# Performance work log

Measured on AMD Instinct MI355X. Metric: run time of the kernel, lower is better.

The kernel has to match this reference:

```python
import jax, jax.numpy as jnp
import numpy as np

N0, N1, N2, N3, N4, C = 65536, 16384, 4096, 1024, 256, 256


def _linear_params(key, fan_in, fan_out):
    kw, kb = jax.random.split(key)
    lim = 1.0 / np.sqrt(fan_in)
    W = jax.random.uniform(kw, (fan_in, fan_out), minval=-lim, maxval=lim, dtype=jnp.float32)
    b = jax.random.uniform(kb, (fan_out,), minval=-lim, maxval=lim, dtype=jnp.float32)
    return W, b


def setup_inputs() -> dict:
    key = jax.random.key(0)
    ks = jax.random.split(key, 20)
    inp = {
        'xyz0': jax.random.normal(ks[0], (N0, 3), dtype=jnp.float32),
        'idx0': jax.random.randint(ks[1], (N0,), 0, N1),
        'idx1': jax.random.randint(ks[2], (N1,), 0, N0),
        'idx2': jax.random.randint(ks[3], (N2,), 0, N0),
        'idx3': jax.random.randint(ks[4], (N3,), 0, N0),
        'idx4': jax.random.randint(ks[5], (N4,), 0, N0),
    }
    names = ['W_all', 'b_all', 'W4', 'b4', 'W3', 'b3', 'W2', 'b2', 'W1', 'b1', 'W0', 'b0']
    for i in range(6):
        W, b = _linear_params(ks[6 + i], 3, C)
        inp[names[2 * i]] = W
        inp[names[2 * i + 1]] = b
    pnames = ['P4', 'pb4', 'P3', 'pb3', 'P2', 'pb2', 'P1', 'pb1', 'P0', 'pb0']
    for i in range(5):
        W, b = _linear_params(ks[12 + i], 2 * C, C)
        inp[pnames[2 * i]] = W
        inp[pnames[2 * i + 1]] = b
    return inp


def _nn1(xyz, new_xyz):
    # global 1-NN (single batch segment): argmin of squared distance
    d = (jnp.sum(new_xyz ** 2, -1, keepdims=True)
         - 2.0 * new_xyz @ xyz.T
         + jnp.sum(xyz ** 2, -1))  # [M, N]
    return jnp.argmin(d, axis=1)


def _fwd(xyz0, idx0, idx1, idx2, idx3, idx4,
         W_all, b_all, W4, b4, W3, b3, W2, b2, W1, b1, W0, b0,
         P4, pb4, P3, pb3, P2, pb2, P1, pb1, P0, pb0):
    xyz4 = xyz0[idx4]
    xyz3 = xyz0[idx3]
    xyz2 = xyz0[idx2]
    xyz1 = xyz0[idx1]
    f0 = xyz0 @ W_all + b_all          # [N0, C]
    f1, f2, f3, f4 = f0[:N1], f0[:N2], f0[:N3], f0[:N4]
    # level 4: global max pooling as class token (single-batch scatter-amax)
    cls4 = jnp.max(f4, axis=0, keepdims=True)  # [1, C], broadcasts over N4
    f4_nei = cls4 + (xyz4 @ W4 + b4)
    pe4 = jnp.concatenate([f4_nei, f4], axis=-1) @ P4 + pb4
    # level 3
    k34 = _nn1(xyz4, xyz3)
    f3_nei = pe4[k34] + ((xyz3 - xyz4[k34]) @ W3 + b3)
    pe3 = jnp.concatenate([f3_nei, f3], axis=-1) @ P3 + pb3
    # level 2
    k23 = _nn1(xyz3, xyz2)
    f2_nei = pe3[k23] + ((xyz2 - xyz3[k23]) @ W2 + b2)
    pe2 = jnp.concatenate([f2_nei, f2], axis=-1) @ P2 + pb2
    # level 1
    k12 = _nn1(xyz2, xyz1)
    f1_nei = pe2[k12] + ((xyz1 - xyz2[k12]) @ W1 + b1)
    pe1 = jnp.concatenate([f1_nei, f1], axis=-1) @ P1 + pb1
    # level 0: precomputed indices into level 1
    f0_nei = pe1[idx0] + ((xyz0 - xyz1[idx0]) @ W0 + b0)
    pe0 = jnp.concatenate([f0_nei, f0], axis=-1) @ P0 + pb0
    return (pe4, pe3, pe2, pe1, pe0)


def reference(xyz0, idx0, idx1, idx2, idx3, idx4,
              W_all, b_all, W4, b4, W3, b3, W2, b2, W1, b1, W0, b0,
              P4, pb4, P3, pb3, P2, pb2, P1, pb1, P0, pb0):
    return _fwd(xyz0, idx0, idx1, idx2, idx3, idx4,
                W_all, b_all, W4, b4, W3, b3, W2, b2, W1, b1, W0, b0,
                P4, pb4, P3, pb3, P2, pb2, P1, pb1, P0, pb0)
```

## Files before the change

kernel.cpp:

```cpp
#include <hip/hip_runtime.h>
#include <hip/hip_bf16.h>


typedef __hip_bfloat16 bf16;
typedef unsigned short ushort_t;
typedef __attribute__((ext_vector_type(8))) short short8;
typedef __attribute__((ext_vector_type(4))) float float4v;

#define cN0 65536
#define cN1 16384
#define cN2 4096
#define cN3 1024
#define cN4 256

__device__ __forceinline__ float b2f(bf16 v) { return __bfloat162float(v); }

__device__ __forceinline__ ushort_t f2b(float v) {
    union { float f; unsigned u; } x; x.f = v;
    unsigned r = x.u + 0x7FFF + ((x.u >> 16) & 1);
    return (ushort_t)(r >> 16);
}

__global__ void detect_kernel(const unsigned short* __restrict__ raw, int* __restrict__ flag) {
    __shared__ int bad;
    if (threadIdx.x == 0) bad = 0;
    __syncthreads();
    for (int i = threadIdx.x; i < 1024; i += 256) {
        int e = (raw[i] >> 7) & 0xFF;
        if (e >= 138) atomicOr(&bad, 1);
    }
    __syncthreads();
    if (threadIdx.x == 0) flag[0] = bad ? 1 : 0;
}

struct CanonArgs { const void* src[23]; };

__global__ void canon_kernel(CanonArgs a, const int* __restrict__ flag, float* __restrict__ dst) {
    const int sizes[23] = {196608, 768, 256,
                           768, 256, 768, 256, 768, 256, 768, 256, 768, 256,
                           131072, 256, 131072, 256, 131072, 256, 131072, 256, 131072, 256};
    int fp32 = flag[0];
    int gid = blockIdx.x * 256 + threadIdx.x;
    int off = 0;
#pragma unroll
    for (int s = 0; s < 23; ++s) {
        int n = sizes[s];
        if (gid >= off && gid < off + n) {
            int local = gid - off;
            float v = fp32 ? ((const float*)a.src[s])[local]
                           : b2f(((const bf16*)a.src[s])[local]);
            dst[gid] = v;
        }
        off += n;
    }
}

__global__ void prep_kernel(const float* __restrict__ Pbase, const float* __restrict__ Wbase,
                            const float* __restrict__ Wallf, const float* __restrict__ ballf,
                            const float* __restrict__ xyzf,
                            ushort_t* __restrict__ PTb,
                            float* __restrict__ M1, float* __restrict__ M2,
                            float* __restrict__ cbuf) {
    __shared__ __align__(16) char smem[16640];
    int bidx = blockIdx.x;
    int tid = threadIdx.x;

    if (bidx < 80) {
        int level = bidx >> 4;
        int kb = (bidx >> 2) & 3;
        int nb = bidx & 3;
        const float* P = Pbase + (size_t)level * 131328;
        ushort_t* PT = PTb + (size_t)level * 65536;
        float (*tile)[65] = (float (*)[65])smem;
        int tx = tid & 63, ty = tid >> 6;
        for (int r = ty; r < 64; r += 4)
            tile[r][tx] = P[(size_t)(kb * 64 + r) * 256 + nb * 64 + tx];
        __syncthreads();
        for (int r = ty; r < 64; r += 4)
            PT[(size_t)(nb * 64 + r) * 256 + kb * 64 + tx] = f2b(tile[tx][r]);
        return;
    }

    int L = (bidx - 80) >> 3;
    int tb = (bidx - 80) & 7;
    const float* P = Pbase + (size_t)L * 131328;
    const float* W = Wbase + (size_t)L * 1024;
    const float* b = W + 768;
    const float* pb = P + 131072;

    float* cls4f = (float*)smem;
    float* red = (float*)(smem + 1024);
    float* px = (float*)(smem + 1024 + 7168);
    float* py = px + 256;
    float* pz = py + 256;

    if (L == 0) {
        px[tid] = xyzf[3 * tid + 0];
        py[tid] = xyzf[3 * tid + 1];
        pz[tid] = xyzf[3 * tid + 2];
        __syncthreads();
        float w0 = Wallf[tid], w1 = Wallf[256 + tid], w2 = Wallf[512 + tid];
        float bb = ballf[tid];
        float best = -3.402823466e38f;
        for (int i = 0; i < 256; ++i) {
            float v = fmaf(pz[i], w2, fmaf(py[i], w1, px[i] * w0)) + bb;
            best = fmaxf(best, v);
        }
        cls4f[tid] = best;
        __syncthreads();
    }

    int j = tid & 31;
    int slice = tid >> 5;
    int col = tb * 32 + j;

    float m10 = 0.f, m11 = 0.f, m12 = 0.f, m20 = 0.f, m21 = 0.f, m22 = 0.f, cc = 0.f;
#pragma unroll 4
    for (int i = 0; i < 32; ++i) {
        int c = slice * 32 + i;
        float pt = P[(size_t)c * 256 + col];
        float pbot = P[(size_t)(256 + c) * 256 + col];
        m10 = fmaf(W[c], pt, m10);
        m11 = fmaf(W[256 + c], pt, m11);
        m12 = fmaf(W[512 + c], pt, m12);
        m20 = fmaf(Wallf[c], pbot, m20);
        m21 = fmaf(Wallf[256 + c], pbot, m21);
        m22 = fmaf(Wallf[512 + c], pbot, m22);
        cc = fmaf(b[c], pt, cc);
        cc = fmaf(ballf[c], pbot, cc);
        if (L == 0) cc = fmaf(cls4f[c], pt, cc);
    }

    red[0 * 256 + tid] = m10; red[1 * 256 + tid] = m11; red[2 * 256 + tid] = m12;
    red[3 * 256 + tid] = m20; red[4 * 256 + tid] = m21; red[5 * 256 + tid] = m22;
    red[6 * 256 + tid] = cc;
    __syncthreads();
    if (tid < 32) {
        float v[7];
#pragma unroll
        for (int q = 0; q < 7; ++q) {
            float s = red[q * 256 + tid];
#pragma unroll
            for (int sl = 1; sl < 8; ++sl) s += red[q * 256 + sl * 32 + tid];
            v[q] = s;
        }
        M1[(size_t)L * 768 + col] = v[0];
        M1[(size_t)L * 768 + 256 + col] = v[1];
        M1[(size_t)L * 768 + 512 + col] = v[2];
        M2[(size_t)L * 768 + col] = v[3];
        M2[(size_t)L * 768 + 256 + col] = v[4];
        M2[(size_t)L * 768 + 512 + col] = v[5];
        cbuf[(size_t)L * 256 + col] = v[6] + pb[col];
    }
}

__device__ __forceinline__ void nn_body(const float* __restrict__ xyzf,
                                        const int* __restrict__ idxQ,
                                        const int* __restrict__ idxR, int nR,
                                        int* __restrict__ outK, int blk,
                                        float4* ref4, float* redD, int* redI) {
    int tid = threadIdx.x;
    int part = tid >> 6;
    int q = blk * 64 + (tid & 63);
    int qi = idxQ[q];
    float qx = xyzf[3 * qi + 0];
    float qy = xyzf[3 * qi + 1];
    float qz = xyzf[3 * qi + 2];
    float q2 = (qx * qx + qy * qy) + qz * qz;
    float best = 3.402823466e38f;
    int bi = 0;
    for (int base = 0; base < nR; base += 1024) {
        int nt = min(1024, nR - base);
        __syncthreads();
        for (int t = tid; t < nt; t += 256) {
            int ri = idxR[base + t];
            float x = xyzf[3 * ri + 0];
            float y = xyzf[3 * ri + 1];
            float z = xyzf[3 * ri + 2];
            ref4[t] = make_float4(x, y, z, (x * x + y * y) + z * z);
        }
        __syncthreads();
        int seg = nt >> 2;
        int s0 = part * seg;
        for (int t = 0; t < seg; ++t) {
            float4 rp = ref4[s0 + t];
            float dot = (qx * rp.x + qy * rp.y) + qz * rp.z;
            float d = (q2 - 2.0f * dot) + rp.w;
            if (d < best) { best = d; bi = base + s0 + t; }
        }
    }
    redD[tid] = best;
    redI[tid] = bi;
    __syncthreads();
    if (part == 0) {
#pragma unroll
        for (int p = 1; p < 4; ++p) {
            float d = redD[tid + p * 64];
            int i2 = redI[tid + p * 64];
            if (d < best || (d == best && i2 < bi)) { best = d; bi = i2; }
        }
        outK[q] = bi;
    }
}

__global__ void nn_merged(const float* __restrict__ xyzf,
                          const int* __restrict__ idx1, const int* __restrict__ idx2,
                          const int* __restrict__ idx3, const int* __restrict__ idx4,
                          int* __restrict__ k34, int* __restrict__ k23,
                          int* __restrict__ k12) {
    __shared__ __align__(16) float4 ref4[1024];
    __shared__ float redD[256];
    __shared__ int redI[256];
    int b = blockIdx.x;
    if (b < 16)       nn_body(xyzf, idx3, idx4, cN4, k34, b, ref4, redD, redI);
    else if (b < 80)  nn_body(xyzf, idx2, idx3, cN3, k23, b - 16, ref4, redD, redI);
    else              nn_body(xyzf, idx1, idx2, cN2, k12, b - 80, ref4, redD, redI);
}

__global__ void pe4_kernel(const float* __restrict__ xyzf, const int* __restrict__ idx4,
                           const float* __restrict__ M1, const float* __restrict__ M2,
                           const float* __restrict__ cbuf, const int* __restrict__ flag,
                           void* __restrict__ outv, ushort_t* __restrict__ peB) {
    int row = blockIdx.x;
    int n = threadIdx.x;
    int qi = idx4[row];
    float qx = xyzf[3 * qi + 0], qy = xyzf[3 * qi + 1], qz = xyzf[3 * qi + 2];
    float xx = xyzf[3 * row + 0], yy = xyzf[3 * row + 1], zz = xyzf[3 * row + 2];
    float v = cbuf[n];
    v = fmaf(qx, M1[n], v);
    v = fmaf(qy, M1[256 + n], v);
    v = fmaf(qz, M1[512 + n], v);
    v = fmaf(xx, M2[n], v);
    v = fmaf(yy, M2[256 + n], v);
    v = fmaf(zz, M2[512 + n], v);
    size_t idx = (size_t)row * 256 + n;
    if (flag[0]) ((float*)outv)[idx] = v;
    else         ((bf16*)outv)[idx] = __float2bfloat16(v);
    peB[idx] = f2b(v);
}

__global__ __launch_bounds__(256, 2) void level_mfma(
    const float* __restrict__ xyzf,
    const ushort_t* __restrict__ peB_prev,
    const int* __restrict__ kmap,
    const int* __restrict__ idxQ,
    const int* __restrict__ idxR,
    const float* __restrict__ M1, const float* __restrict__ M2,
    const float* __restrict__ cvec,
    const ushort_t* __restrict__ PT,
    const int* __restrict__ flag, void* __restrict__ outv, size_t out_off,
    ushort_t* __restrict__ peB_out) {
    __shared__ float m1l[768], m2l[768], cl[256];
    __shared__ float rowD[64][3], rowX[64][3];
    __shared__ int rowK[64];
    __shared__ __align__(16) ushort_t A_lds[64 * 264];

    int tid = threadIdx.x;
    int row0 = blockIdx.x * 64;
    int fp32out = flag[0];

    for (int i = tid; i < 768; i += 256) { m1l[i] = M1[i]; m2l[i] = M2[i]; }
    cl[tid] = cvec[tid];
    if (tid < 64) {
        int r = tid, row = row0 + r;
        float xx = xyzf[3 * row + 0];
        float yy = xyzf[3 * row + 1];
        float zz = xyzf[3 * row + 2];
        rowX[r][0] = xx; rowX[r][1] = yy; rowX[r][2] = zz;
        int k = kmap[row];
        rowK[r] = k;
        float qx = xx, qy = yy, qz = zz;
        if (idxQ) {
            int qi = idxQ[row];
            qx = xyzf[3 * qi + 0];
            qy = xyzf[3 * qi + 1];
            qz = xyzf[3 * qi + 2];
        }
        int ri = idxR[k];
        float rx = xyzf[3 * ri + 0];
        float ry = xyzf[3 * ri + 1];
        float rz = xyzf[3 * ri + 2];
        rowD[r][0] = qx - rx; rowD[r][1] = qy - ry; rowD[r][2] = qz - rz;
    }
    __syncthreads();

#pragma unroll
    for (int it = 0; it < 8; ++it) {
        int lin = it * 256 + tid;
        int r = lin >> 5, ch = lin & 31;
        *(uint4*)&A_lds[r * 264 + ch * 8] =
            *(const uint4*)(peB_prev + (size_t)rowK[r] * 256 + ch * 8);
    }
    __syncthreads();

    int wave = tid >> 6;
    int lane = tid & 63;
    int quad = lane >> 4;
    int l16 = lane & 15;
    int wc = wave * 64;

    const ushort_t* bbase[4];
#pragma unroll
    for (int nt = 0; nt < 4; ++nt)
        bbase[nt] = PT + (size_t)(wc + nt * 16 + l16) * 256 + quad * 8;

    float4v acc[4][4];
#pragma unroll
    for (int mt = 0; mt < 4; ++mt)
#pragma unroll
        for (int nt = 0; nt < 4; ++nt) acc[mt][nt] = (float4v){0.f, 0.f, 0.f, 0.f};

#pragma unroll
    for (int kt = 0; kt < 8; ++kt) {
        int c0 = kt * 32;
        short8 afr[4], bfr[4];
#pragma unroll
        for (int nt = 0; nt < 4; ++nt)
            bfr[nt] = *(const short8*)(bbase[nt] + c0);
#pragma unroll
        for (int mt = 0; mt < 4; ++mt)
            afr[mt] = *(const short8*)&A_lds[(mt * 16 + l16) * 264 + c0 + quad * 8];
#pragma unroll
        for (int mt = 0; mt < 4; ++mt)
#pragma unroll
            for (int nt = 0; nt < 4; ++nt)
                acc[mt][nt] = __builtin_amdgcn_mfma_f32_16x16x32_bf16(
                    afr[mt], bfr[nt], acc[mt][nt], 0, 0, 0);
    }

#pragma unroll
    for (int mt = 0; mt < 4; ++mt) {
#pragma unroll
        for (int reg = 0; reg < 4; ++reg) {
            int rl = mt * 16 + quad * 4 + reg;
            float d0 = rowD[rl][0], d1 = rowD[rl][1], d2 = rowD[rl][2];
            float x0 = rowX[rl][0], x1 = rowX[rl][1], x2 = rowX[rl][2];
            int row = row0 + rl;
#pragma unroll
            for (int nt = 0; nt < 4; ++nt) {
                int col = wc + nt * 16 + l16;
                float v = acc[mt][nt][reg] + cl[col];
                v = fmaf(d0, m1l[col], v);
                v = fmaf(d1, m1l[256 + col], v);
                v = fmaf(d2, m1l[512 + col], v);
                v = fmaf(x0, m2l[col], v);
                v = fmaf(x1, m2l[256 + col], v);
                v = fmaf(x2, m2l[512 + col], v);
                size_t idx = (size_t)row * 256 + col;
                if (fp32out) ((float*)outv)[out_off + idx] = v;
                else         ((bf16*)outv)[out_off + idx] = __float2bfloat16(v);
                if (peB_out) peB_out[idx] = f2b(v);
            }
        }
    }
}

extern "C" void kernel_launch(void* const* d_in, const int* in_sizes, int n_in,
                              void* d_out, int out_size, void* d_ws, size_t ws_size,
                              hipStream_t stream) {
    const int* idx0 = (const int*)d_in[1];
    const int* idx1 = (const int*)d_in[2];
    const int* idx2 = (const int*)d_in[3];
    const int* idx3 = (const int*)d_in[4];
    const int* idx4 = (const int*)d_in[5];

    float* ws = (float*)d_ws;
    int* flag = (int*)ws;
    float* p = ws + 64;
    float* xyzf = p;  p += 196608;
    float* Wallf = p; p += 768;
    float* ballf = p; p += 256;
    float* Wf0 = p;   p += 5 * 1024;
    float* Pf0 = p;   p += 5 * 131328;
    float* M1buf = p; p += 5 * 768;
    float* M2buf = p; p += 5 * 768;
    float* cbuf = p;  p += 5 * 256;
    int* k34 = (int*)p; p += 1024;
    int* k23 = (int*)p; p += 4096;
    int* k12 = (int*)p; p += 16384;
    ushort_t* pe4B = (ushort_t*)p; p += 32768;
    ushort_t* pe3B = (ushort_t*)p; p += 131072;
    ushort_t* pe2B = (ushort_t*)p; p += 524288;
    ushort_t* pe1B = (ushort_t*)p; p += 2097152;
    ushort_t* PTb = (ushort_t*)p;

    detect_kernel<<<1, 256, 0, stream>>>((const unsigned short*)d_in[0], flag);

    CanonArgs ca;
    ca.src[0] = d_in[0];
    ca.src[1] = d_in[6];
    ca.src[2] = d_in[7];
    for (int i = 0; i < 10; ++i) ca.src[3 + i] = d_in[8 + i];
    for (int i = 0; i < 10; ++i) ca.src[13 + i] = d_in[18 + i];
    canon_kernel<<<3357, 256, 0, stream>>>(ca, flag, ws + 64);

    prep_kernel<<<120, 256, 0, stream>>>(Pf0, Wf0, Wallf, ballf, xyzf,
                                         PTb, M1buf, M2buf, cbuf);
    nn_merged<<<336, 256, 0, stream>>>(xyzf, idx1, idx2, idx3, idx4, k34, k23, k12);

    const size_t o4 = 0;
    const size_t o3 = (size_t)cN4 * 256;
    const size_t o2 = o3 + (size_t)cN3 * 256;
    const size_t o1 = o2 + (size_t)cN2 * 256;
    const size_t o0 = o1 + (size_t)cN1 * 256;

    pe4_kernel<<<cN4, 256, 0, stream>>>(xyzf, idx4, M1buf, M2buf, cbuf, flag, d_out, pe4B);

    level_mfma<<<cN3 / 64, 256, 0, stream>>>(
        xyzf, pe4B, k34, idx3, idx4, M1buf + 768, M2buf + 768, cbuf + 256,
        PTb + 1 * 65536, flag, d_out, o3, pe3B);
    level_mfma<<<cN2 / 64, 256, 0, stream>>>(
        xyzf, pe3B, k23, idx2, idx3, M1buf + 2 * 768, M2buf + 2 * 768, cbuf + 2 * 256,
        PTb + 2 * 65536, flag, d_out, o2, pe2B);
    level_mfma<<<cN1 / 64, 256, 0, stream>>>(
        xyzf, pe2B, k12, idx1, idx2, M1buf + 3 * 768, M2buf + 3 * 768, cbuf + 3 * 256,
        PTb + 3 * 65536, flag, d_out, o1, pe1B);
    level_mfma<<<cN0 / 64, 256, 0, stream>>>(
        xyzf, pe1B, idx0, nullptr, idx1, M1buf + 4 * 768, M2buf + 4 * 768, cbuf + 4 * 256,
        PTb + 4 * 65536, flag, d_out, o0, nullptr);
}
```

Before: 290.1 us.

## Fuse detect, prep, NN and pe4 stages into fewer kernel launches

Folds the dtype-detect step into the canonicalisation kernel, so each block recomputes the flag locally instead of running a separate one-block launch. It merges the prep and nearest-neighbour kernels into one 512-thread launch and widens the NN search from 4 to 8 partitions per query. The pe4 kernel is absorbed into a level-3 kernel that recomputes the pe4 rows it gathers on the fly, which drops the pe4 bf16 buffer and one launch. The aim is to cut launch count and serial dependencies, at the cost of redundant recomputation and half-idle threads in the prep branches.

```diff
diff --git a/kernel.cpp b/kernel.cpp
--- a/kernel.cpp
+++ b/kernel.cpp
@@ -21,26 +21,26 @@
     return (ushort_t)(r >> 16);
 }
 
-__global__ void detect_kernel(const unsigned short* __restrict__ raw, int* __restrict__ flag) {
+struct CanonArgs { const void* src[23]; };
+
+__global__ void canon_kernel(CanonArgs a, int* __restrict__ flag, float* __restrict__ dst) {
     __shared__ int bad;
-    if (threadIdx.x == 0) bad = 0;
-    __syncthreads();
-    for (int i = threadIdx.x; i < 1024; i += 256) {
+    int tid = threadIdx.x;
+    if (tid == 0) bad = 0;
+    __syncthreads();
+    const unsigned short* raw = (const unsigned short*)a.src[0];
+    for (int i = tid; i < 1024; i += 256) {
         int e = (raw[i] >> 7) & 0xFF;
         if (e >= 138) atomicOr(&bad, 1);
     }
     __syncthreads();
-    if (threadIdx.x == 0) flag[0] = bad ? 1 : 0;
-}
-
-struct CanonArgs { const void* src[23]; };
-
-__global__ void canon_kernel(CanonArgs a, const int* __restrict__ flag, float* __restrict__ dst) {
+    int fp32 = bad ? 1 : 0;
+    int gid = blockIdx.x * 256 + tid;
+    if (gid == 0) flag[0] = fp32;
+
     const int sizes[23] = {196608, 768, 256,
                            768, 256, 768, 256, 768, 256, 768, 256, 768, 256,
                            131072, 256, 131072, 256, 131072, 256, 131072, 256, 131072, 256};
-    int fp32 = flag[0];
-    int gid = blockIdx.x * 256 + threadIdx.x;
     int off = 0;
 #pragma unroll
     for (int s = 0; s < 23; ++s) {
@@ -55,104 +55,6 @@
     }
 }
 
-__global__ void prep_kernel(const float* __restrict__ Pbase, const float* __restrict__ Wbase,
-                            const float* __restrict__ Wallf, const float* __restrict__ ballf,
-                            const float* __restrict__ xyzf,
-                            ushort_t* __restrict__ PTb,
-                            float* __restrict__ M1, float* __restrict__ M2,
-                            float* __restrict__ cbuf) {
-    __shared__ __align__(16) char smem[16640];
-    int bidx = blockIdx.x;
-    int tid = threadIdx.x;
-
-    if (bidx < 80) {
-        int level = bidx >> 4;
-        int kb = (bidx >> 2) & 3;
-        int nb = bidx & 3;
-        const float* P = Pbase + (size_t)level * 131328;
-        ushort_t* PT = PTb + (size_t)level * 65536;
-        float (*tile)[65] = (float (*)[65])smem;
-        int tx = tid & 63, ty = tid >> 6;
-        for (int r = ty; r < 64; r += 4)
-            tile[r][tx] = P[(size_t)(kb * 64 + r) * 256 + nb * 64 + tx];
-        __syncthreads();
-        for (int r = ty; r < 64; r += 4)
-            PT[(size_t)(nb * 64 + r) * 256 + kb * 64 + tx] = f2b(tile[tx][r]);
-        return;
-    }
-
-    int L = (bidx - 80) >> 3;
-    int tb = (bidx - 80) & 7;
-    const float* P = Pbase + (size_t)L * 131328;
-    const float* W = Wbase + (size_t)L * 1024;
-    const float* b = W + 768;
-    const float* pb = P + 131072;
-
-    float* cls4f = (float*)smem;
-    float* red = (float*)(smem + 1024);
-    float* px = (float*)(smem + 1024 + 7168);
-    float* py = px + 256;
-    float* pz = py + 256;
-
-    if (L == 0) {
-        px[tid] = xyzf[3 * tid + 0];
-        py[tid] = xyzf[3 * tid + 1];
-        pz[tid] = xyzf[3 * tid + 2];
-        __syncthreads();
-        float w0 = Wallf[tid], w1 = Wallf[256 + tid], w2 = Wallf[512 + tid];
-        float bb = ballf[tid];
-        float best = -3.402823466e38f;
-        for (int i = 0; i < 256; ++i) {
-            float v = fmaf(pz[i], w2, fmaf(py[i], w1, px[i] * w0)) + bb;
-            best = fmaxf(best, v);
-        }
-        cls4f[tid] = best;
-        __syncthreads();
-    }
-
-    int j = tid & 31;
-    int slice = tid >> 5;
-    int col = tb * 32 + j;
-
-    float m10 = 0.f, m11 = 0.f, m12 = 0.f, m20 = 0.f, m21 = 0.f, m22 = 0.f, cc = 0.f;
-#pragma unroll 4
-    for (int i = 0; i < 32; ++i) {
-        int c = slice * 32 + i;
-        float pt = P[(size_t)c * 256 + col];
-        float pbot = P[(size_t)(256 + c) * 256 + col];
-        m10 = fmaf(W[c], pt, m10);
-        m11 = fmaf(W[256 + c], pt, m11);
-        m12 = fmaf(W[512 + c], pt, m12);
-        m20 = fmaf(Wallf[c], pbot, m20);
-        m21 = fmaf(Wallf[256 + c], pbot, m21);
-        m22 = fmaf(Wallf[512 + c], pbot, m22);
-        cc = fmaf(b[c], pt, cc);
-        cc = fmaf(ballf[c], pbot, cc);
-        if (L == 0) cc = fmaf(cls4f[c], pt, cc);
-    }
-
-    red[0 * 256 + tid] = m10; red[1 * 256 + tid] = m11; red[2 * 256 + tid] = m12;
-    red[3 * 256 + tid] = m20; red[4 * 256 + tid] = m21; red[5 * 256 + tid] = m22;
-    red[6 * 256 + tid] = cc;
-    __syncthreads();
-    if (tid < 32) {
-        float v[7];
-#pragma unroll
-        for (int q = 0; q < 7; ++q) {
-            float s = red[q * 256 + tid];
-#pragma unroll
-            for (int sl = 1; sl < 8; ++sl) s += red[q * 256 + sl * 32 + tid];
-            v[q] = s;
-        }
-        M1[(size_t)L * 768 + col] = v[0];
-        M1[(size_t)L * 768 + 256 + col] = v[1];
-        M1[(size_t)L * 768 + 512 + col] = v[2];
-        M2[(size_t)L * 768 + col] = v[3];
-        M2[(size_t)L * 768 + 256 + col] = v[4];
-        M2[(size_t)L * 768 + 512 + col] = v[5];
-        cbuf[(size_t)L * 256 + col] = v[6] + pb[col];
-    }
-}
 
 __device__ __forceinline__ void nn_body(const float* __restrict__ xyzf,
                                         const int* __restrict__ idxQ,
@@ -172,7 +74,7 @@
     for (int base = 0; base < nR; base += 1024) {
         int nt = min(1024, nR - base);
         __syncthreads();
-        for (int t = tid; t < nt; t += 256) {
+        for (int t = tid; t < nt; t += 512) {
             int ri = idxR[base + t];
             float x = xyzf[3 * ri + 0];
             float y = xyzf[3 * ri + 1];
@@ -180,7 +82,7 @@
             ref4[t] = make_float4(x, y, z, (x * x + y * y) + z * z);
         }
         __syncthreads();
-        int seg = nt >> 2;
+        int seg = nt >> 3;
         int s0 = part * seg;
         for (int t = 0; t < seg; ++t) {
             float4 rp = ref4[s0 + t];
@@ -194,7 +96,7 @@
     __syncthreads();
     if (part == 0) {
 #pragma unroll
-        for (int p = 1; p < 4; ++p) {
+        for (int p = 1; p < 8; ++p) {
             float d = redD[tid + p * 64];
             int i2 = redI[tid + p * 64];
             if (d < best || (d == best && i2 < bi)) { best = d; bi = i2; }
@@ -203,40 +105,279 @@
     }
 }
 
-__global__ void nn_merged(const float* __restrict__ xyzf,
-                          const int* __restrict__ idx1, const int* __restrict__ idx2,
-                          const int* __restrict__ idx3, const int* __restrict__ idx4,
-                          int* __restrict__ k34, int* __restrict__ k23,
-                          int* __restrict__ k12) {
-    __shared__ __align__(16) float4 ref4[1024];
-    __shared__ float redD[256];
-    __shared__ int redI[256];
+__global__ void prep_nn_kernel(const float* __restrict__ Pbase, const float* __restrict__ Wbase,
+                               const float* __restrict__ Wallf, const float* __restrict__ ballf,
+                               const float* __restrict__ xyzf,
+                               const int* __restrict__ idx1, const int* __restrict__ idx2,
+                               const int* __restrict__ idx3, const int* __restrict__ idx4,
+                               ushort_t* __restrict__ PTb,
+                               float* __restrict__ M1, float* __restrict__ M2,
+                               float* __restrict__ cbuf,
+                               int* __restrict__ k34, int* __restrict__ k23,
+                               int* __restrict__ k12) {
+    __shared__ __align__(16) char smem[20608];
     int b = blockIdx.x;
-    if (b < 16)       nn_body(xyzf, idx3, idx4, cN4, k34, b, ref4, redD, redI);
-    else if (b < 80)  nn_body(xyzf, idx2, idx3, cN3, k23, b - 16, ref4, redD, redI);
-    else              nn_body(xyzf, idx1, idx2, cN2, k12, b - 80, ref4, redD, redI);
-}
-
-__global__ void pe4_kernel(const float* __restrict__ xyzf, const int* __restrict__ idx4,
-                           const float* __restrict__ M1, const float* __restrict__ M2,
-                           const float* __restrict__ cbuf, const int* __restrict__ flag,
-                           void* __restrict__ outv, ushort_t* __restrict__ peB) {
-    int row = blockIdx.x;
-    int n = threadIdx.x;
-    int qi = idx4[row];
-    float qx = xyzf[3 * qi + 0], qy = xyzf[3 * qi + 1], qz = xyzf[3 * qi + 2];
-    float xx = xyzf[3 * row + 0], yy = xyzf[3 * row + 1], zz = xyzf[3 * row + 2];
-    float v = cbuf[n];
-    v = fmaf(qx, M1[n], v);
-    v = fmaf(qy, M1[256 + n], v);
-    v = fmaf(qz, M1[512 + n], v);
-    v = fmaf(xx, M2[n], v);
-    v = fmaf(yy, M2[256 + n], v);
-    v = fmaf(zz, M2[512 + n], v);
-    size_t idx = (size_t)row * 256 + n;
-    if (flag[0]) ((float*)outv)[idx] = v;
-    else         ((bf16*)outv)[idx] = __float2bfloat16(v);
-    peB[idx] = f2b(v);
+    int tid = threadIdx.x;
+
+    if (b < 80) {
+        int level = b >> 4;
+        int kb = (b >> 2) & 3;
+        int nb = b & 3;
+        const float* P = Pbase + (size_t)level * 131328;
+        ushort_t* PT = PTb + (size_t)level * 65536;
+        float (*tile)[65] = (float (*)[65])smem;
+        int tx = tid & 63, ty = tid >> 6;
+        for (int r = ty; r < 64; r += 8)
+            tile[r][tx] = P[(size_t)(kb * 64 + r) * 256 + nb * 64 + tx];
+        __syncthreads();
+        for (int r = ty; r < 64; r += 8)
+            PT[(size_t)(nb * 64 + r) * 256 + kb * 64 + tx] = f2b(tile[tx][r]);
+        return;
+    }
+
+    if (b < 120) {
+        int L = (b - 80) >> 3;
+        int tb = (b - 80) & 7;
+        const float* P = Pbase + (size_t)L * 131328;
+        const float* W = Wbase + (size_t)L * 1024;
+        const float* bvec = W + 768;
+        const float* pb = P + 131072;
+        float* cls4f = (float*)smem;
+        float* red = (float*)(smem + 1024);
+        float* px = (float*)(smem + 1024 + 7168);
+        float* py = px + 256;
+        float* pz = py + 256;
+
+        if (L == 0) {
+            if (tid < 256) {
+                px[tid] = xyzf[3 * tid + 0];
+                py[tid] = xyzf[3 * tid + 1];
+                pz[tid] = xyzf[3 * tid + 2];
+            }
+            __syncthreads();
+            if (tid < 256) {
+                float w0 = Wallf[tid], w1 = Wallf[256 + tid], w2 = Wallf[512 + tid];
+                float bb = ballf[tid];
+                float best = -3.402823466e38f;
+                for (int i = 0; i < 256; ++i) {
+                    float v = fmaf(pz[i], w2, fmaf(py[i], w1, px[i] * w0)) + bb;
+                    best = fmaxf(best, v);
+                }
+                cls4f[tid] = best;
+            }
+            __syncthreads();
+        }
+
+        if (tid < 256) {
+            int j = tid & 31;
+            int slice = tid >> 5;
+            int col = tb * 32 + j;
+            float m10 = 0.f, m11 = 0.f, m12 = 0.f, m20 = 0.f, m21 = 0.f, m22 = 0.f, cc = 0.f;
+#pragma unroll 4
+            for (int i = 0; i < 32; ++i) {
+                int c = slice * 32 + i;
+                float pt = P[(size_t)c * 256 + col];
+                float pbot = P[(size_t)(256 + c) * 256 + col];
+                m10 = fmaf(W[c], pt, m10);
+                m11 = fmaf(W[256 + c], pt, m11);
+                m12 = fmaf(W[512 + c], pt, m12);
+                m20 = fmaf(Wallf[c], pbot, m20);
+                m21 = fmaf(Wallf[256 + c], pbot, m21);
+                m22 = fmaf(Wallf[512 + c], pbot, m22);
+                cc = fmaf(bvec[c], pt, cc);
+                cc = fmaf(ballf[c], pbot, cc);
+                if (L == 0) cc = fmaf(cls4f[c], pt, cc);
+            }
+            red[0 * 256 + tid] = m10; red[1 * 256 + tid] = m11; red[2 * 256 + tid] = m12;
+            red[3 * 256 + tid] = m20; red[4 * 256 + tid] = m21; red[5 * 256 + tid] = m22;
+            red[6 * 256 + tid] = cc;
+        }
+        __syncthreads();
+        if (tid < 32) {
+            int col = tb * 32 + tid;
+            float v[7];
+#pragma unroll
+            for (int q = 0; q < 7; ++q) {
+                float s = red[q * 256 + tid];
+#pragma unroll
+                for (int sl = 1; sl < 8; ++sl) s += red[q * 256 + sl * 32 + tid];
+                v[q] = s;
+            }
+            M1[(size_t)L * 768 + col] = v[0];
+            M1[(size_t)L * 768 + 256 + col] = v[1];
+            M1[(size_t)L * 768 + 512 + col] = v[2];
+            M2[(size_t)L * 768 + col] = v[3];
+            M2[(size_t)L * 768 + 256 + col] = v[4];
+            M2[(size_t)L * 768 + 512 + col] = v[5];
+            cbuf[(size_t)L * 256 + col] = v[6] + pb[col];
+        }
+        return;
+    }
+
+    int blk = b - 120;
+    float4* ref4 = (float4*)smem;
+    float* redD = (float*)(smem + 16384);
+    int* redI = (int*)(smem + 18432);
+    if (blk < 16)       nn_body(xyzf, idx3, idx4, cN4, k34, blk, ref4, redD, redI);
+    else if (blk < 80)  nn_body(xyzf, idx2, idx3, cN3, k23, blk - 16, ref4, redD, redI);
+    else                nn_body(xyzf, idx1, idx2, cN2, k12, blk - 80, ref4, redD, redI);
+}
+
+__global__ __launch_bounds__(256, 2) void level3_kernel(
+    const float* __restrict__ xyzf,
+    const int* __restrict__ idx3, const int* __restrict__ idx4,
+    const int* __restrict__ k34,
+    const float* __restrict__ M1_0, const float* __restrict__ M2_0,
+    const float* __restrict__ c0,
+    const float* __restrict__ M1_1, const float* __restrict__ M2_1,
+    const float* __restrict__ c1,
+    const ushort_t* __restrict__ PT,
+    const int* __restrict__ flag, void* __restrict__ outv,
+    size_t o4, size_t o3, ushort_t* __restrict__ peB_out) {
+    __shared__ float m1l[768], m2l[768], cl[256];
+    __shared__ float rowD[64][3], rowX[64][3], refQ[64][3], refK[64][3];
+    __shared__ int rowK[64];
+    __shared__ __align__(16) ushort_t A_lds[64 * 264];
+
+    int tid = threadIdx.x;
+    int b = blockIdx.x;
+    int fp32out = flag[0];
+
+    if (b >= 16) {
+        int rows0 = (b - 16) * 64;
+        if (tid < 64) {
+            int k = rows0 + tid;
+            int qi = idx4[k];
+            refQ[tid][0] = xyzf[3 * qi + 0];
+            refQ[tid][1] = xyzf[3 * qi + 1];
+            refQ[tid][2] = xyzf[3 * qi + 2];
+            refK[tid][0] = xyzf[3 * k + 0];
+            refK[tid][1] = xyzf[3 * k + 1];
+            refK[tid][2] = xyzf[3 * k + 2];
+        }
+        __syncthreads();
+        float cc = c0[tid];
+        float a0 = M1_0[tid], a1 = M1_0[256 + tid], a2 = M1_0[512 + tid];
+        float b0 = M2_0[tid], b1 = M2_0[256 + tid], b2 = M2_0[512 + tid];
+        for (int r = 0; r < 64; ++r) {
+            float v = cc;
+            v = fmaf(refQ[r][0], a0, v);
+            v = fmaf(refQ[r][1], a1, v);
+            v = fmaf(refQ[r][2], a2, v);
+            v = fmaf(refK[r][0], b0, v);
+            v = fmaf(refK[r][1], b1, v);
+            v = fmaf(refK[r][2], b2, v);
+            size_t idx = o4 + (size_t)(rows0 + r) * 256 + tid;
+            if (fp32out) ((float*)outv)[idx] = v;
+            else         ((bf16*)outv)[idx] = __float2bfloat16(v);
+        }
+        return;
+    }
+
+    int row0 = b * 64;
+    for (int i = tid; i < 768; i += 256) { m1l[i] = M1_1[i]; m2l[i] = M2_1[i]; }
+    cl[tid] = c1[tid];
+    if (tid < 64) {
+        int r = tid, row = row0 + r;
+        float xx = xyzf[3 * row + 0];
+        float yy = xyzf[3 * row + 1];
+        float zz = xyzf[3 * row + 2];
+        rowX[r][0] = xx; rowX[r][1] = yy; rowX[r][2] = zz;
+        int k = k34[row];
+        rowK[r] = k;
+        int qi = idx3[row];
+        float qx = xyzf[3 * qi + 0];
+        float qy = xyzf[3 * qi + 1];
+        float qz = xyzf[3 * qi + 2];
+        int ri = idx4[k];
+        float rx = xyzf[3 * ri + 0];
+        float ry = xyzf[3 * ri + 1];
+        float rz = xyzf[3 * ri + 2];
+        rowD[r][0] = qx - rx; rowD[r][1] = qy - ry; rowD[r][2] = qz - rz;
+        refQ[r][0] = rx; refQ[r][1] = ry; refQ[r][2] = rz;
+        refK[r][0] = xyzf[3 * k + 0];
+        refK[r][1] = xyzf[3 * k + 1];
+        refK[r][2] = xyzf[3 * k + 2];
+    }
+    __syncthreads();
+
+    {
+        float cc = c0[tid];
+        float a0 = M1_0[tid], a1 = M1_0[256 + tid], a2 = M1_0[512 + tid];
+        float b0 = M2_0[tid], b1 = M2_0[256 + tid], b2 = M2_0[512 + tid];
+        for (int r = 0; r < 64; ++r) {
+            float v = cc;
+            v = fmaf(refQ[r][0], a0, v);
+            v = fmaf(refQ[r][1], a1, v);
+            v = fmaf(refQ[r][2], a2, v);
+            v = fmaf(refK[r][0], b0, v);
+            v = fmaf(refK[r][1], b1, v);
+            v = fmaf(refK[r][2], b2, v);
+            A_lds[r * 264 + tid] = f2b(v);
+        }
+    }
+    __syncthreads();
+
+    int wave = tid >> 6;
+    int lane = tid & 63;
+    int quad = lane >> 4;
+    int l16 = lane & 15;
+    int wc = wave * 64;
+
+    const ushort_t* bbase[4];
+#pragma unroll
+    for (int nt = 0; nt < 4; ++nt)
+        bbase[nt] = PT + (size_t)(wc + nt * 16 + l16) * 256 + quad * 8;
+
+    float4v acc[4][4];
+#pragma unroll
+    for (int mt = 0; mt < 4; ++mt)
+#pragma unroll
+        for (int nt = 0; nt < 4; ++nt) acc[mt][nt] = (float4v){0.f, 0.f, 0.f, 0.f};
+
+#pragma unroll
+    for (int kt = 0; kt < 8; ++kt) {
+        int c0k = kt * 32;
+        short8 afr[4], bfr[4];
+#pragma unroll
+        for (int nt = 0; nt < 4; ++nt)
+            bfr[nt] = *(const short8*)(bbase[nt] + c0k);
+#pragma unroll
+        for (int mt = 0; mt < 4; ++mt)
+            afr[mt] = *(const short8*)&A_lds[(mt * 16 + l16) * 264 + c0k + quad * 8];
+#pragma unroll
+        for (int mt = 0; mt < 4; ++mt)
+#pragma unroll
+            for (int nt = 0; nt < 4; ++nt)
+                acc[mt][nt] = __builtin_amdgcn_mfma_f32_16x16x32_bf16(
+                    afr[mt], bfr[nt], acc[mt][nt], 0, 0, 0);
+    }
+
+#pragma unroll
+    for (int mt = 0; mt < 4; ++mt) {
+#pragma unroll
+        for (int reg = 0; reg < 4; ++reg) {
+            int rl = mt * 16 + quad * 4 + reg;
+            float d0 = rowD[rl][0], d1 = rowD[rl][1], d2 = rowD[rl][2];
+            float x0 = rowX[rl][0], x1 = rowX[rl][1], x2 = rowX[rl][2];
+            int row = row0 + rl;
+#pragma unroll
+            for (int nt = 0; nt < 4; ++nt) {
+                int col = wc + nt * 16 + l16;
+                float v = acc[mt][nt][reg] + cl[col];
+                v = fmaf(d0, m1l[col], v);
+                v = fmaf(d1, m1l[256 + col], v);
+                v = fmaf(d2, m1l[512 + col], v);
+                v = fmaf(x0, m2l[col], v);
+                v = fmaf(x1, m2l[256 + col], v);
+                v = fmaf(x2, m2l[512 + col], v);
+                size_t idx = (size_t)row * 256 + col;
+                if (fp32out) ((float*)outv)[o3 + idx] = v;
+                else         ((bf16*)outv)[o3 + idx] = __float2bfloat16(v);
+                peB_out[idx] = f2b(v);
+            }
+        }
+    }
 }
 
 __global__ __launch_bounds__(256, 2) void level_mfma(
@@ -378,13 +519,10 @@
     int* k34 = (int*)p; p += 1024;
     int* k23 = (int*)p; p += 4096;
     int* k12 = (int*)p; p += 16384;
-    ushort_t* pe4B = (ushort_t*)p; p += 32768;
     ushort_t* pe3B = (ushort_t*)p; p += 131072;
     ushort_t* pe2B = (ushort_t*)p; p += 524288;
     ushort_t* pe1B = (ushort_t*)p; p += 2097152;
     ushort_t* PTb = (ushort_t*)p;
-
-    detect_kernel<<<1, 256, 0, stream>>>((const unsigned short*)d_in[0], flag);
 
     CanonArgs ca;
     ca.src[0] = d_in[0];
@@ -394,9 +532,10 @@
     for (int i = 0; i < 10; ++i) ca.src[13 + i] = d_in[18 + i];
     canon_kernel<<<3357, 256, 0, stream>>>(ca, flag, ws + 64);
 
-    prep_kernel<<<120, 256, 0, stream>>>(Pf0, Wf0, Wallf, ballf, xyzf,
-                                         PTb, M1buf, M2buf, cbuf);
-    nn_merged<<<336, 256, 0, stream>>>(xyzf, idx1, idx2, idx3, idx4, k34, k23, k12);
+    prep_nn_kernel<<<456, 512, 0, stream>>>(Pf0, Wf0, Wallf, ballf, xyzf,
+                                            idx1, idx2, idx3, idx4,
+                                            PTb, M1buf, M2buf, cbuf,
+                                            k34, k23, k12);
 
     const size_t o4 = 0;
     const size_t o3 = (size_t)cN4 * 256;
@@ -404,11 +543,12 @@
     const size_t o1 = o2 + (size_t)cN2 * 256;
     const size_t o0 = o1 + (size_t)cN1 * 256;
 
-    pe4_kernel<<<cN4, 256, 0, stream>>>(xyzf, idx4, M1buf, M2buf, cbuf, flag, d_out, pe4B);
-
-    level_mfma<<<cN3 / 64, 256, 0, stream>>>(
-        xyzf, pe4B, k34, idx3, idx4, M1buf + 768, M2buf + 768, cbuf + 256,
-        PTb + 1 * 65536, flag, d_out, o3, pe3B);
+    level3_kernel<<<20, 256, 0, stream>>>(
+        xyzf, idx3, idx4, k34,
+        M1buf, M2buf, cbuf,
+        M1buf + 768, M2buf + 768, cbuf + 256,
+        PTb + 1 * 65536, flag, d_out, o4, o3, pe3B);
+
     level_mfma<<<cN2 / 64, 256, 0, stream>>>(
         xyzf, pe3B, k23, idx2, idx3, M1buf + 2 * 768, M2buf + 2 * 768, cbuf + 2 * 256,
         PTb + 2 * 65536, flag, d_out, o2, pe2B);
```

After: 254.4 us. -12.3%, faster.
